# Optimization experiments

Hardware: AMD Instinct MI355X
Metric: run time of the kernel (lower is better)

## Reference

```python
import jax, jax.numpy as jnp
import numpy as np

M, K, N = 16384, 2048, 2048

def setup_inputs() -> dict:
    key = jax.random.key(0)
    k1, k2 = jax.random.split(key)
    # int8 activations and int8 weights in [-127, 127)
    x = jax.random.randint(k1, (M, K), -127, 127, dtype=jnp.int32).astype(jnp.int8)
    weight = jax.random.randint(k2, (K, N), -127, 127, dtype=jnp.int32).astype(jnp.int8)
    bias = jnp.zeros((N,), dtype=jnp.float16)
    return {"x": x, "weight": weight, "bias": bias}

def reference(x, weight, bias):
    # then fused bias add in floating point.
    acc = jax.lax.dot_general(
        x, weight,
        dimension_numbers=(((1,), (0,)), ((), ())),
        preferred_element_type=jnp.int32,
    )  # [M, N] int32
    out = acc.astype(jnp.float32) + bias.astype(jnp.float32)
    return out
```

## Files before the change

### kernel.cpp

```cpp
#include <hip/hip_runtime.h>
#include <hip/hip_fp16.h>

#define M_DIM 16384
#define K_DIM 2048
#define N_DIM 2048

#define BM 128
#define BN 128
#define BK 64

typedef int int4v  __attribute__((ext_vector_type(4)));
typedef int int16v __attribute__((ext_vector_type(16)));

__device__ __forceinline__ void gl_lds16(const void* g, void* l) {
    __builtin_amdgcn_global_load_lds(
        (const __attribute__((address_space(1))) void*)g,
        (__attribute__((address_space(3))) void*)l,
        16, 0, 0);
}

__device__ __forceinline__ int pack4(int4v v) {
    return (v[0] & 255) | ((v[1] & 255) << 8) | ((v[2] & 255) << 16) | (v[3] << 24);
}

__global__ void pack_x_kernel(const int* __restrict__ x, char* __restrict__ xp) {
    int i = blockIdx.x * 256 + threadIdx.x;
    const int4v* src = (const int4v*)x;
    int4v a = src[i * 4 + 0];
    int4v b = src[i * 4 + 1];
    int4v c = src[i * 4 + 2];
    int4v d = src[i * 4 + 3];
    int4v o;
    o[0] = pack4(a); o[1] = pack4(b); o[2] = pack4(c); o[3] = pack4(d);
    ((int4v*)xp)[i] = o;
}

__global__ void wt_pack_kernel(const int* __restrict__ w, char* __restrict__ wt) {
    __shared__ char tile[64][68];
    int b  = blockIdx.x;
    int k0 = (b & 31) * 64;
    int n0 = (b >> 5) * 64;
    int t  = threadIdx.x;
    int r  = t >> 2;
    int c  = (t & 3) * 16;

    const int* src = w + (size_t)(k0 + r) * N_DIM + n0 + c;
    int4v a = *(const int4v*)(src + 0);
    int4v bb = *(const int4v*)(src + 4);
    int4v cc = *(const int4v*)(src + 8);
    int4v dd = *(const int4v*)(src + 12);
    *(int*)&tile[r][c + 0]  = pack4(a);
    *(int*)&tile[r][c + 4]  = pack4(bb);
    *(int*)&tile[r][c + 8]  = pack4(cc);
    *(int*)&tile[r][c + 12] = pack4(dd);
    __syncthreads();

    char buf[16];
#pragma unroll
    for (int j = 0; j < 16; ++j) buf[j] = tile[c + j][r];
    *(int4v*)(wt + (size_t)(n0 + r) * K_DIM + k0 + c) = *(int4v*)buf;
}

__global__ void gemm_i8_kernel(const char* __restrict__ A, const char* __restrict__ BT,
                               const __half* __restrict__ bias, float* __restrict__ C) {
    __shared__ char Asm[BM * BK];
    __shared__ char Bsm[BN * BK];

    int bid = blockIdx.x;
    int mt = bid & 127;
    int nt = bid >> 7;
    int R0 = mt * BM, C0 = nt * BN;

    int t = threadIdx.x;
    int lane = t & 63;
    int w = t >> 6;
    int wm = w & 1, wn = w >> 1;

    int16v acc[2][2];
#pragma unroll
    for (int i = 0; i < 2; ++i)
#pragma unroll
        for (int j = 0; j < 2; ++j) acc[i][j] = (int16v)0;

    int s0 = t, s1 = t + 256;
    int r5_0 = s0 & 31, kh0 = (s0 >> 5) & 1, ks0 = (s0 >> 6) & 1, mb0 = s0 >> 7;
    int r5_1 = s1 & 31, kh1 = (s1 >> 5) & 1, ks1 = (s1 >> 6) & 1, mb1 = s1 >> 7;
    size_t aoff0 = (size_t)(R0 + mb0 * 32 + r5_0) * K_DIM + (ks0 * 32 + kh0 * 16);
    size_t aoff1 = (size_t)(R0 + mb1 * 32 + r5_1) * K_DIM + (ks1 * 32 + kh1 * 16);
    size_t boff0 = (size_t)(C0 + mb0 * 32 + r5_0) * K_DIM + (ks0 * 32 + kh0 * 16);
    size_t boff1 = (size_t)(C0 + mb1 * 32 + r5_1) * K_DIM + (ks1 * 32 + kh1 * 16);

    for (int it = 0; it < K_DIM / BK; ++it) {
        int k0 = it * BK;
        gl_lds16(A + aoff0 + k0, &Asm[s0 * 16]);
        gl_lds16(A + aoff1 + k0, &Asm[s1 * 16]);
        gl_lds16(BT + boff0 + k0, &Bsm[s0 * 16]);
        gl_lds16(BT + boff1 + k0, &Bsm[s1 * 16]);
        __syncthreads();

#pragma unroll
        for (int ks = 0; ks < 2; ++ks) {
            int4v af[2], bf[2];
#pragma unroll
            for (int i = 0; i < 2; ++i)
                af[i] = *(const int4v*)&Asm[(((wm * 2 + i) * 2 + ks) * 64 + lane) * 16];
#pragma unroll
            for (int j = 0; j < 2; ++j)
                bf[j] = *(const int4v*)&Bsm[(((wn * 2 + j) * 2 + ks) * 64 + lane) * 16];
#pragma unroll
            for (int i = 0; i < 2; ++i)
#pragma unroll
                for (int j = 0; j < 2; ++j)
                    acc[i][j] = __builtin_amdgcn_mfma_i32_32x32x32_i8(af[i], bf[j], acc[i][j], 0, 0, 0);
        }
        __syncthreads();
    }

    int col = lane & 31;
    int rbase = (lane >> 5) * 4;
#pragma unroll
    for (int j = 0; j < 2; ++j) {
        int cn = C0 + wn * 64 + j * 32 + col;
        float bv = __half2float(bias[cn]);
#pragma unroll
        for (int i = 0; i < 2; ++i) {
            int rm = R0 + wm * 64 + i * 32 + rbase;
#pragma unroll
            for (int reg = 0; reg < 16; ++reg) {
                int row = rm + (reg & 3) + 8 * (reg >> 2);
                C[(size_t)row * N_DIM + cn] = (float)acc[i][j][reg] + bv;
            }
        }
    }
}

extern "C" void kernel_launch(void* const* d_in, const int* in_sizes, int n_in,
                              void* d_out, int out_size, void* d_ws, size_t ws_size,
                              hipStream_t stream) {
    const int* x = (const int*)d_in[0];
    const int* wgt = (const int*)d_in[1];
    const __half* bias = (const __half*)d_in[2];
    float* out = (float*)d_out;

    char* xp = (char*)d_ws;
    char* wt = (char*)d_ws + (size_t)M_DIM * K_DIM;

    pack_x_kernel<<<(M_DIM * (size_t)K_DIM) / 16 / 256, 256, 0, stream>>>(x, xp);
    wt_pack_kernel<<<(K_DIM / 64) * (N_DIM / 64), 256, 0, stream>>>(wgt, wt);
    gemm_i8_kernel<<<(M_DIM / BM) * (N_DIM / BN), 256, 0, stream>>>(xp, wt, bias, out);
}
```

Baseline: 363.0 us.

## Pre-tile operands into MFMA-ready blocks and widen GEMM tile to 128x256

The pack kernels now write A and B^T in a blocked layout: for each 32-row block and each 64-wide K segment, 2048 contiguous bytes arranged exactly as the LDS fragments expect. Each GEMM K-step therefore loads contiguous chunks with simple offsets instead of strided rows. The GEMM tile grows from 128x128 to 128x256 with 512 threads and launch bounds, which halves how often A is re-read and raises work per block. The cost is more LDS per block and fewer blocks in the grid, which may reduce occupancy.

```diff
diff --git a/kernel.cpp b/kernel.cpp
--- a/kernel.cpp
+++ b/kernel.cpp
@@ -4,9 +4,10 @@
 #define M_DIM 16384
 #define K_DIM 2048
 #define N_DIM 2048
+#define KSEG  (K_DIM / 64)
 
 #define BM 128
-#define BN 128
+#define BN 256
 #define BK 64
 
 typedef int int4v  __attribute__((ext_vector_type(4)));
@@ -23,19 +24,21 @@
     return (v[0] & 255) | ((v[1] & 255) << 8) | ((v[2] & 255) << 16) | (v[3] << 24);
 }
 
-__global__ void pack_x_kernel(const int* __restrict__ x, char* __restrict__ xp) {
-    int i = blockIdx.x * 256 + threadIdx.x;
-    const int4v* src = (const int4v*)x;
-    int4v a = src[i * 4 + 0];
-    int4v b = src[i * 4 + 1];
-    int4v c = src[i * 4 + 2];
-    int4v d = src[i * 4 + 3];
+
+__global__ void pack_x_kernel(const int* __restrict__ x, char* __restrict__ at) {
+    int t = threadIdx.x;
+    int u = blockIdx.x * 2 + (t >> 7);
+    int tt = t & 127;
+    int mblk = u >> 5, kseg = u & 31;
+    int r = tt & 31;
+    int kin = ((tt >> 5) & 3) * 16;
+    const int4v* src = (const int4v*)(x + (size_t)(mblk * 32 + r) * K_DIM + kseg * 64 + kin);
     int4v o;
-    o[0] = pack4(a); o[1] = pack4(b); o[2] = pack4(c); o[3] = pack4(d);
-    ((int4v*)xp)[i] = o;
+    o[0] = pack4(src[0]); o[1] = pack4(src[1]); o[2] = pack4(src[2]); o[3] = pack4(src[3]);
+    ((int4v*)at)[blockIdx.x * 256 + t] = o;
 }
 
-__global__ void wt_pack_kernel(const int* __restrict__ w, char* __restrict__ wt) {
+__global__ void wt_pack_kernel(const int* __restrict__ w, char* __restrict__ bt) {
     __shared__ char tile[64][68];
     int b  = blockIdx.x;
     int k0 = (b & 31) * 64;
@@ -58,11 +61,16 @@
     char buf[16];
 #pragma unroll
     for (int j = 0; j < 16; ++j) buf[j] = tile[c + j][r];
-    *(int4v*)(wt + (size_t)(n0 + r) * K_DIM + k0 + c) = *(int4v*)buf;
+    int n = n0 + r;
+    int nblk = n >> 5, r31 = n & 31;
+    int kseg = k0 >> 6;
+    int sl = (c >> 4) * 32 + r31;
+    *(int4v*)(bt + ((size_t)(nblk * KSEG + kseg) * 128 + sl) * 16) = *(int4v*)buf;
 }
 
-__global__ void gemm_i8_kernel(const char* __restrict__ A, const char* __restrict__ BT,
-                               const __half* __restrict__ bias, float* __restrict__ C) {
+__global__ __launch_bounds__(512, 4)
+void gemm_i8_kernel(const char* __restrict__ A, const char* __restrict__ BT,
+                    const __half* __restrict__ bias, float* __restrict__ C) {
     __shared__ char Asm[BM * BK];
     __shared__ char Bsm[BN * BK];
 
@@ -82,20 +90,15 @@
 #pragma unroll
         for (int j = 0; j < 2; ++j) acc[i][j] = (int16v)0;
 
-    int s0 = t, s1 = t + 256;
-    int r5_0 = s0 & 31, kh0 = (s0 >> 5) & 1, ks0 = (s0 >> 6) & 1, mb0 = s0 >> 7;
-    int r5_1 = s1 & 31, kh1 = (s1 >> 5) & 1, ks1 = (s1 >> 6) & 1, mb1 = s1 >> 7;
-    size_t aoff0 = (size_t)(R0 + mb0 * 32 + r5_0) * K_DIM + (ks0 * 32 + kh0 * 16);
-    size_t aoff1 = (size_t)(R0 + mb1 * 32 + r5_1) * K_DIM + (ks1 * 32 + kh1 * 16);
-    size_t boff0 = (size_t)(C0 + mb0 * 32 + r5_0) * K_DIM + (ks0 * 32 + kh0 * 16);
-    size_t boff1 = (size_t)(C0 + mb1 * 32 + r5_1) * K_DIM + (ks1 * 32 + kh1 * 16);
+    unsigned abase  = (unsigned)((R0 >> 5) + (t >> 7)) * (KSEG * 2048) + (t & 127) * 16;
+    unsigned bbase0 = (unsigned)((C0 >> 5) + (t >> 7)) * (KSEG * 2048) + (t & 127) * 16;
+    unsigned bbase1 = (unsigned)((C0 >> 5) + (t >> 7) + 4) * (KSEG * 2048) + (t & 127) * 16;
 
     for (int it = 0; it < K_DIM / BK; ++it) {
-        int k0 = it * BK;
-        gl_lds16(A + aoff0 + k0, &Asm[s0 * 16]);
-        gl_lds16(A + aoff1 + k0, &Asm[s1 * 16]);
-        gl_lds16(BT + boff0 + k0, &Bsm[s0 * 16]);
-        gl_lds16(BT + boff1 + k0, &Bsm[s1 * 16]);
+        unsigned ko = it * 2048;
+        gl_lds16(A + abase + ko,   &Asm[t * 16]);
+        gl_lds16(BT + bbase0 + ko, &Bsm[t * 16]);
+        gl_lds16(BT + bbase1 + ko, &Bsm[(t + 512) * 16]);
         __syncthreads();
 
 #pragma unroll
@@ -142,10 +145,10 @@
     const __half* bias = (const __half*)d_in[2];
     float* out = (float*)d_out;
 
-    char* xp = (char*)d_ws;
-    char* wt = (char*)d_ws + (size_t)M_DIM * K_DIM;
+    char* at = (char*)d_ws;
+    char* bt = (char*)d_ws + (size_t)M_DIM * K_DIM;
 
-    pack_x_kernel<<<(M_DIM * (size_t)K_DIM) / 16 / 256, 256, 0, stream>>>(x, xp);
-    wt_pack_kernel<<<(K_DIM / 64) * (N_DIM / 64), 256, 0, stream>>>(wgt, wt);
-    gemm_i8_kernel<<<(M_DIM / BM) * (N_DIM / BN), 256, 0, stream>>>(xp, wt, bias, out);
+    pack_x_kernel<<<(M_DIM / 32) * KSEG / 2, 256, 0, stream>>>(x, at);
+    wt_pack_kernel<<<(K_DIM / 64) * (N_DIM / 64), 256, 0, stream>>>(wgt, bt);
+    gemm_i8_kernel<<<(M_DIM / BM) * (N_DIM / BN), 512, 0, stream>>>(at, bt, bias, out);
 }
```

Result: faster. 314.2 us (-13.4%).
